# Kernel optimization log

Hardware: AMD Instinct MI355X
Metric: run time of the kernel (lower is better)

The kernel has to match this reference:

```python
import jax, jax.numpy as jnp
import numpy as np

EPS = 1e-5
H = 16  # num_heads


def _ln(x, s, b):
    m = x.mean(-1, keepdims=True)
    v = x.var(-1, keepdims=True)
    return (x - m) / jnp.sqrt(v + EPS) * s + b


def _gru_gate(x, y, W, U, bg):
    # W, U: [3, D, D] stacked (Wr, Wz, Wg) / (Ur, Uz, Ug); torch Linear: a @ W.T
    r = jax.nn.sigmoid(y @ W[0].T + x @ U[0].T)
    z = jax.nn.sigmoid(y @ W[1].T + x @ U[1].T - bg)
    h = jnp.tanh(y @ W[2].T + (r * x) @ U[2].T)
    return (1.0 - z) * x + z * h


def setup_inputs() -> dict:
    N, L, D = 4, 1024, 1024
    hs = D // H
    rng = jax.random.key(0)
    ks = iter(jax.random.split(rng, 24))

    def xav(shape):
        sc = float(np.sqrt(2.0 / (shape[-1] + shape[-2])))
        return jax.random.normal(next(ks), shape, jnp.float32) * sc

    inp = {
        'value': jax.random.normal(next(ks), (N, L, D), jnp.float32),
        'key': jax.random.normal(next(ks), (N, L, D), jnp.float32),
        'query': jax.random.normal(next(ks), (N, L, D), jnp.float32),
        'mask': jax.random.randint(next(ks), (N, L), 0, 2).astype(jnp.int32),
        # shared-head QKV projections (head_size x head_size)
        'wq': xav((hs, hs)), 'wk': xav((hs, hs)), 'wv': xav((hs, hs)),
        'w_out': xav((D, D)), 'b_out': jnp.zeros((D,), jnp.float32),
        'fc_w': xav((D, D)), 'fc_b': jnp.zeros((D,), jnp.float32),
        'ln1_s': jnp.ones((D,), jnp.float32), 'ln1_b': jnp.zeros((D,), jnp.float32),
        'lnkv_s': jnp.ones((D,), jnp.float32), 'lnkv_b': jnp.zeros((D,), jnp.float32),
        'ln2_s': jnp.ones((D,), jnp.float32), 'ln2_b': jnp.zeros((D,), jnp.float32),
        'g1_W': xav((3, D, D)), 'g1_U': xav((3, D, D)), 'g1_bg': jnp.full((D,), 2.0, jnp.float32),
        'g2_W': xav((3, D, D)), 'g2_U': xav((3, D, D)), 'g2_bg': jnp.full((D,), 2.0, jnp.float32),
    }
    return inp


def reference(value, key, query, mask, wq, wk, wv, w_out, b_out, fc_w, fc_b,
              ln1_s, ln1_b, lnkv_s, lnkv_b, ln2_s, ln2_b,
              g1_W, g1_U, g1_bg, g2_W, g2_U, g2_bg):
    N, L, D = query.shape
    hs = D // H
    # pre-LN: query normed with norm1, value normed with norm_kv; key := normed value
    q_ = _ln(query, ln1_s, ln1_b)
    v_ = _ln(value, lnkv_s, lnkv_b)
    k_ = v_
    # shared per-head projections: [N, L, H, hs] @ W.T
    qh = q_.reshape(N, L, H, hs) @ wq.T
    kh = k_.reshape(N, L, H, hs) @ wk.T
    vh = v_.reshape(N, L, H, hs) @ wv.T
    energy = jnp.einsum('nqhd,nkhd->nhqk', qh, kh)
    energy = jnp.where(mask[:, None, None, :] == 0, jnp.float32(-1e20), energy)
    # NOTE: original scales by sqrt(embed_dim), not sqrt(head_size)
    attn = jax.nn.softmax(energy / jnp.sqrt(jnp.float32(D)), axis=-1)
    o = jnp.einsum('nhqk,nkhd->nqhd', attn, vh).reshape(N, L, D) @ w_out.T + b_out
    # GRU-gated residuals (GTrXL)
    h = _gru_gate(query, o, g1_W, g1_U, g1_bg)
    h_ = _ln(h, ln2_s, ln2_b)
    f = jax.nn.relu(h_ @ fc_w.T + fc_b)
    out = _gru_gate(h, f, g2_W, g2_U, g2_bg)
    return out, attn
```

## Files before the change

kernel.cpp:

```cpp
#include <hip/hip_runtime.h>
#include <cstdint>
#include <cstddef>

#define N_ 4
#define L_ 1024
#define D_ 1024
#define H_ 16
#define HS_ 64
#define M_ (N_*L_)
#define DD_ (D_*D_)
#define MD_ ((size_t)M_*D_)

typedef unsigned short u16;
typedef __bf16 b16x8 __attribute__((ext_vector_type(8)));
typedef float f32x4 __attribute__((ext_vector_type(4)));

__device__ __forceinline__ float sigmoidf_(float x) { return 1.0f / (1.0f + __expf(-x)); }
__device__ __forceinline__ u16 f2bf(float f) {
    union { float f; uint32_t u; } c; c.f = f;
    uint32_t u = c.u;
    u += 0x7fffu + ((u >> 16) & 1u);
    return (u16)(u >> 16);
}

template<int AUX>
__device__ __forceinline__ void gl_lds16(const void* g, void* l) {
    auto gp = reinterpret_cast<const __attribute__((address_space(1))) unsigned int*>(
        reinterpret_cast<uintptr_t>(g));
    auto lp = reinterpret_cast<__attribute__((address_space(3))) unsigned int*>(
        reinterpret_cast<uintptr_t>(l));
    __builtin_amdgcn_global_load_lds(gp, lp, 16, 0, AUX);
}

__global__ __launch_bounds__(256) void prep_weights_kernel(
    const float* __restrict__ w_out, const float* __restrict__ fc_w,
    const float* __restrict__ wq, const float* __restrict__ wk, const float* __restrict__ wv,
    const float* __restrict__ g1W, const float* __restrict__ g1U,
    const float* __restrict__ g2W, const float* __restrict__ g2U,
    const float* __restrict__ query, u16* __restrict__ Xq,
    u16* __restrict__ ws0) {
    u16* Wop = ws0;
    u16* Wfc = ws0 + (size_t)DD_;
    u16* WQKV = ws0 + 2 * (size_t)DD_;
    u16* G1rz = WQKV + 16384;
    u16* G1h = G1rz + 4 * (size_t)DD_;
    u16* G2rz = G1h + 2 * (size_t)DD_;
    u16* G2h = G2rz + 4 * (size_t)DD_;
    int b = blockIdx.x, t = threadIdx.x;
    const float* src; u16* dst; size_t si, di;
    if (b < 512) {
        size_t f = (size_t)b * 2048 + t * 8; src = w_out; si = f; dst = Wop; di = f;
    } else if (b < 1024) {
        size_t f = (size_t)(b - 512) * 2048 + t * 8; src = fc_w; si = f; dst = Wfc; di = f;
    } else if (b < 1030) {
        size_t f = (size_t)(b - 1024) * 2048 + t * 8;
        int which = (int)(f >> 12); size_t off = f & 4095;
        src = which == 0 ? wq : (which == 1 ? wk : wv); si = off; dst = WQKV; di = f;
    } else if (b < 3078) {
        size_t f = (size_t)(b - 1030) * 2048 + t * 8;
        size_t row = f >> 11, k = f & 2047; size_t n2 = (row >= 1024) ? 1 : 0;
        src = (k < 1024) ? (g1W + n2 * DD_) : (g1U + n2 * DD_);
        si = (row & 1023) * 1024 + (k & 1023); dst = G1rz; di = f;
    } else if (b < 4102) {
        size_t f = (size_t)(b - 3078) * 2048 + t * 8;
        size_t row = f >> 11, k = f & 2047;
        src = (k < 1024) ? (g1W + 2 * (size_t)DD_) : (g1U + 2 * (size_t)DD_);
        si = row * 1024 + (k & 1023); dst = G1h; di = f;
    } else if (b < 6150) {
        size_t f = (size_t)(b - 4102) * 2048 + t * 8;
        size_t row = f >> 11, k = f & 2047; size_t n2 = (row >= 1024) ? 1 : 0;
        src = (k < 1024) ? (g2W + n2 * DD_) : (g2U + n2 * DD_);
        si = (row & 1023) * 1024 + (k & 1023); dst = G2rz; di = f;
    } else if (b < 7174) {
        size_t f = (size_t)(b - 6150) * 2048 + t * 8;
        size_t row = f >> 11, k = f & 2047;
        src = (k < 1024) ? (g2W + 2 * (size_t)DD_) : (g2U + 2 * (size_t)DD_);
        si = row * 1024 + (k & 1023); dst = G2h; di = f;
    } else {
        size_t f = (size_t)(b - 7174) * 2048 + t * 8;
        src = query; si = f; dst = Xq; di = f;
    }
    float4 a = *(const float4*)&src[si];
    float4 b4 = *(const float4*)&src[si + 4];
    u16 o[8] = { f2bf(a.x), f2bf(a.y), f2bf(a.z), f2bf(a.w),
                 f2bf(b4.x), f2bf(b4.y), f2bf(b4.z), f2bf(b4.w) };
    *(uint4*)&dst[di] = *(uint4*)o;
}

__global__ __launch_bounds__(256) void ln2in1_kernel(const float* __restrict__ x0, u16* __restrict__ y0,
                                                     const float* __restrict__ sc0, const float* __restrict__ bi0,
                                                     const float* __restrict__ x1, u16* __restrict__ y1,
                                                     const float* __restrict__ sc1, const float* __restrict__ bi1) {
    int row = blockIdx.x;
    const float* x = blockIdx.y ? x1 : x0;
    u16* y = blockIdx.y ? y1 : y0;
    const float* sc = blockIdx.y ? sc1 : sc0;
    const float* bi = blockIdx.y ? bi1 : bi0;
    const float* xr = x + (size_t)row * D_;
    int t = threadIdx.x;
    float4 v = *(const float4*)&xr[t * 4];
    float s = v.x + v.y + v.z + v.w;
    float q = v.x * v.x + v.y * v.y + v.z * v.z + v.w * v.w;
#pragma unroll
    for (int o = 32; o > 0; o >>= 1) { s += __shfl_xor(s, o); q += __shfl_xor(q, o); }
    __shared__ float ss[4], sq[4];
    int w = t >> 6;
    if ((t & 63) == 0) { ss[w] = s; sq[w] = q; }
    __syncthreads();
    s = ss[0] + ss[1] + ss[2] + ss[3];
    q = sq[0] + sq[1] + sq[2] + sq[3];
    float mean = s * (1.0f / D_);
    float var = q * (1.0f / D_) - mean * mean;
    float inv = rsqrtf(var + 1e-5f);
    float4 sv = *(const float4*)&sc[t * 4];
    float4 bv = *(const float4*)&bi[t * 4];
    u16 ov[4] = { f2bf((v.x - mean) * inv * sv.x + bv.x),
                  f2bf((v.y - mean) * inv * sv.y + bv.y),
                  f2bf((v.z - mean) * inv * sv.z + bv.z),
                  f2bf((v.w - mean) * inv * sv.w + bv.w) };
    *(ushort4*)&y[(size_t)row * D_ + t * 4] = *(ushort4*)ov;
}

__global__ __launch_bounds__(256) void ln_kernel(const float* __restrict__ x, u16* __restrict__ y,
                                                 const float* __restrict__ sc, const float* __restrict__ bi) {
    int row = blockIdx.x;
    const float* xr = x + (size_t)row * D_;
    int t = threadIdx.x;
    float4 v = *(const float4*)&xr[t * 4];
    float s = v.x + v.y + v.z + v.w;
    float q = v.x * v.x + v.y * v.y + v.z * v.z + v.w * v.w;
#pragma unroll
    for (int o = 32; o > 0; o >>= 1) { s += __shfl_xor(s, o); q += __shfl_xor(q, o); }
    __shared__ float ss[4], sq[4];
    int w = t >> 6;
    if ((t & 63) == 0) { ss[w] = s; sq[w] = q; }
    __syncthreads();
    s = ss[0] + ss[1] + ss[2] + ss[3];
    q = sq[0] + sq[1] + sq[2] + sq[3];
    float mean = s * (1.0f / D_);
    float var = q * (1.0f / D_) - mean * mean;
    float inv = rsqrtf(var + 1e-5f);
    float4 sv = *(const float4*)&sc[t * 4];
    float4 bv = *(const float4*)&bi[t * 4];
    u16 ov[4] = { f2bf((v.x - mean) * inv * sv.x + bv.x),
                  f2bf((v.y - mean) * inv * sv.y + bv.y),
                  f2bf((v.z - mean) * inv * sv.z + bv.z),
                  f2bf((v.w - mean) * inv * sv.w + bv.w) };
    *(ushort4*)&y[(size_t)row * D_ + t * 4] = *(ushort4*)ov;
}

__global__ __launch_bounds__(256) void proj_mfma_kernel(const u16* __restrict__ qbf,
                                                        const u16* __restrict__ vbf,
                                                        const u16* __restrict__ wqkv,
                                                        u16* __restrict__ qh, u16* __restrict__ kh,
                                                        u16* __restrict__ vt) {
    int t = threadIdx.x, w = t >> 6, l = t & 63;
    int lr = l & 15, lg = l >> 4;
    int rb = blockIdx.x, h = blockIdx.y;
    int n = rb >> 3, lbase = (rb & 7) * 128;
    const u16* wqp = wqkv;
    const u16* wkp = wqkv + 4096;
    const u16* wvp = wqkv + 8192;
    b16x8 wqf[4][2], wkf[4][2], wvf[4][2];
#pragma unroll
    for (int dt = 0; dt < 4; ++dt)
#pragma unroll
        for (int ks = 0; ks < 2; ++ks) {
            int a = (dt * 16 + lr) * 64 + ks * 32 + lg * 8;
            wqf[dt][ks] = *(const b16x8*)&wqp[a];
            wkf[dt][ks] = *(const b16x8*)&wkp[a];
            wvf[dt][ks] = *(const b16x8*)&wvp[a];
        }
#pragma unroll
    for (int rr = 0; rr < 2; ++rr) {
        int rt = w * 2 + rr;
        size_t grow = (size_t)(n * 1024 + lbase + rt * 16 + lr);
        b16x8 aq[2], av[2];
#pragma unroll
        for (int ks = 0; ks < 2; ++ks) {
            aq[ks] = *(const b16x8*)&qbf[grow * D_ + h * 64 + ks * 32 + lg * 8];
            av[ks] = *(const b16x8*)&vbf[grow * D_ + h * 64 + ks * 32 + lg * 8];
        }
#pragma unroll
        for (int dt = 0; dt < 4; ++dt) {
            f32x4 cq = (f32x4){0.f, 0.f, 0.f, 0.f};
            f32x4 ck = (f32x4){0.f, 0.f, 0.f, 0.f};
            f32x4 cv = (f32x4){0.f, 0.f, 0.f, 0.f};
            cq = __builtin_amdgcn_mfma_f32_16x16x32_bf16(aq[0], wqf[dt][0], cq, 0, 0, 0);
            cq = __builtin_amdgcn_mfma_f32_16x16x32_bf16(aq[1], wqf[dt][1], cq, 0, 0, 0);
            ck = __builtin_amdgcn_mfma_f32_16x16x32_bf16(av[0], wkf[dt][0], ck, 0, 0, 0);
            ck = __builtin_amdgcn_mfma_f32_16x16x32_bf16(av[1], wkf[dt][1], ck, 0, 0, 0);
            cv = __builtin_amdgcn_mfma_f32_16x16x32_bf16(wvf[dt][0], av[0], cv, 0, 0, 0);
            cv = __builtin_amdgcn_mfma_f32_16x16x32_bf16(wvf[dt][1], av[1], cv, 0, 0, 0);
#pragma unroll
            for (int r = 0; r < 4; ++r) {
                size_t orow = (size_t)(n * 1024 + lbase + rt * 16 + lg * 4 + r);
                qh[orow * D_ + h * 64 + dt * 16 + lr] = f2bf(cq[r]);
                kh[orow * D_ + h * 64 + dt * 16 + lr] = f2bf(ck[r]);
                vt[((size_t)(n * H_ + h) * 64 + dt * 16 + lg * 4 + r) * L_ + lbase + rt * 16 + lr] = f2bf(cv[r]);
            }
        }
    }
}

#define PSTR 1032
__global__ __launch_bounds__(512, 4) void qk_pv_kernel(const u16* __restrict__ qh,
                                                       const u16* __restrict__ kh,
                                                       const u16* __restrict__ vt,
                                                       const int* __restrict__ mask,
                                                       float* __restrict__ attn,
                                                       u16* __restrict__ obf) {
    __shared__ u16 P_lds[32 * PSTR];
    __shared__ float redA[32][4];
    __shared__ float redB[32][4];
    int t = threadIdx.x;
    int w = t >> 6, l = t & 63;
    int qsub = w & 1, kq = w >> 1;
    int q0 = blockIdx.x * 32;
    int h = blockIdx.y, n = blockIdx.z;
    int lr = l & 15, lg = l >> 4;

    size_t qrow = ((size_t)(n * L_ + q0 + qsub * 16 + lr) * H_ + h) * HS_;
    b16x8 aq0 = *(const b16x8*)&qh[qrow + lg * 8];
    b16x8 aq1 = *(const b16x8*)&qh[qrow + 32 + lg * 8];

    f32x4 c[16];
#pragma unroll
    for (int i = 0; i < 16; ++i) c[i] = (f32x4){0.f, 0.f, 0.f, 0.f};

    size_t kbase = ((size_t)(n * L_ + kq * 256 + lr) * H_ + h) * HS_ + lg * 8;
#pragma unroll
    for (int kt = 0; kt < 16; ++kt) {
        const u16* kp = &kh[kbase + (size_t)kt * 16 * D_];
        b16x8 bk0 = *(const b16x8*)&kp[0];
        b16x8 bk1 = *(const b16x8*)&kp[32];
        c[kt] = __builtin_amdgcn_mfma_f32_16x16x32_bf16(aq0, bk0, c[kt], 0, 0, 0);
        c[kt] = __builtin_amdgcn_mfma_f32_16x16x32_bf16(aq1, bk1, c[kt], 0, 0, 0);
    }

    const float scl = 0.03125f;
    int kcol = kq * 256 + lr;
    float rowmax[4] = { -1e30f, -1e30f, -1e30f, -1e30f };
#pragma unroll
    for (int kt = 0; kt < 16; ++kt) {
        int mk = mask[n * L_ + kcol + kt * 16];
#pragma unroll
        for (int r = 0; r < 4; ++r) {
            float s = (mk != 0) ? c[kt][r] * scl : -1e20f;
            c[kt][r] = s;
            rowmax[r] = fmaxf(rowmax[r], s);
        }
    }
#pragma unroll
    for (int o = 8; o > 0; o >>= 1)
#pragma unroll
        for (int r = 0; r < 4; ++r) rowmax[r] = fmaxf(rowmax[r], __shfl_xor(rowmax[r], o));

    int qrow4 = qsub * 16 + lg * 4;
    if (lr == 0) {
#pragma unroll
        for (int r = 0; r < 4; ++r) redA[qrow4 + r][kq] = rowmax[r];
    }
    __syncthreads();
#pragma unroll
    for (int r = 0; r < 4; ++r)
        rowmax[r] = fmaxf(fmaxf(redA[qrow4 + r][0], redA[qrow4 + r][1]),
                          fmaxf(redA[qrow4 + r][2], redA[qrow4 + r][3]));
    float rowsum[4] = { 0.f, 0.f, 0.f, 0.f };
#pragma unroll
    for (int kt = 0; kt < 16; ++kt)
#pragma unroll
        for (int r = 0; r < 4; ++r) {
            float e = __expf(c[kt][r] - rowmax[r]);
            c[kt][r] = e;
            rowsum[r] += e;
        }
#pragma unroll
    for (int o = 8; o > 0; o >>= 1)
#pragma unroll
        for (int r = 0; r < 4; ++r) rowsum[r] += __shfl_xor(rowsum[r], o);
    if (lr == 0) {
#pragma unroll
        for (int r = 0; r < 4; ++r) redB[qrow4 + r][kq] = rowsum[r];
    }
    __syncthreads();
    float inv[4];
#pragma unroll
    for (int r = 0; r < 4; ++r)
        inv[r] = 1.0f / (redB[qrow4 + r][0] + redB[qrow4 + r][1] +
                         redB[qrow4 + r][2] + redB[qrow4 + r][3]);

    float* ap = attn + ((size_t)((n * H_ + h) * L_) + q0 + qrow4) * L_ + kcol;
#pragma unroll
    for (int kt = 0; kt < 16; ++kt)
#pragma unroll
        for (int r = 0; r < 4; ++r) {
            float val = c[kt][r] * inv[r];
            __builtin_nontemporal_store(val, &ap[(size_t)r * L_ + kt * 16]);
            P_lds[(size_t)(qrow4 + r) * PSTR + kcol + kt * 16] = f2bf(val);
        }
    __syncthreads();

    int dg = kq;
    const u16* vb = vt + ((size_t)(n * H_ + h) * 64 + dg * 16 + lr) * L_;
    const u16* prow = &P_lds[(size_t)(qsub * 16 + lr) * PSTR];
    f32x4 acc = (f32x4){0.f, 0.f, 0.f, 0.f};
#pragma unroll
    for (int ks = 0; ks < 32; ++ks) {
        b16x8 a = *(const b16x8*)&prow[ks * 32 + lg * 8];
        b16x8 b = *(const b16x8*)&vb[ks * 32 + lg * 8];
        acc = __builtin_amdgcn_mfma_f32_16x16x32_bf16(a, b, acc, 0, 0, 0);
    }
#pragma unroll
    for (int r = 0; r < 4; ++r) {
        size_t q = (size_t)(n * L_ + q0 + qsub * 16 + lg * 4 + r);
        obf[q * D_ + h * 64 + dg * 16 + lr] = f2bf(acc[r]);
    }
}

template<int MODE, int RELU, int WRH>
__global__ __launch_bounds__(512, 4) void gemm_fused_kernel(const u16* __restrict__ A0,
                                                            const u16* __restrict__ A1h,
                                                            const u16* __restrict__ Bw,
                                                            const float* __restrict__ bias,
                                                            const float* __restrict__ xf,
                                                            float* __restrict__ Z,
                                                            u16* __restrict__ Cbf,
                                                            float* __restrict__ outf,
                                                            int K) {
    __shared__ u16 As[2][128 * 64];
    __shared__ u16 Bs[2][128 * 64];
    int t = threadIdx.x, w = t >> 6, l = t & 63;
    int wr = w & 3, wc = w >> 2;
    int flat = blockIdx.x;
    int xcd = flat & 7, idx = flat >> 3;
    int NP = gridDim.x >> 5;
    int ppx = NP >> 3;
    int panel = xcd * ppx + (idx >> 5);
    int mchunk = idx & 31;
    int m0 = mchunk * 128, n0 = panel * 128;
    int fr = l & 15, fq = l >> 4;
    int srow = l >> 3;
    int gc8 = (l & 7) ^ (srow & 7);
    const u16* Bbase = Bw + (size_t)n0 * K;

    f32x4 acc[2][4];
#pragma unroll
    for (int i = 0; i < 2; ++i)
#pragma unroll
        for (int j = 0; j < 4; ++j) acc[i][j] = (f32x4){0.f, 0.f, 0.f, 0.f};

    auto STAGE = [&](int buf, int kk) {
        const u16* Asrc = (MODE == 0 || kk < 1024) ? A0 : A1h;
        int kc = kk & 1023;
#pragma unroll
        for (int i = 0; i < 2; ++i) {
            int r0 = (i * 8 + w) * 8;
            gl_lds16<2>(&Asrc[(size_t)(m0 + r0 + srow) * 1024 + kc + gc8 * 8], &As[buf][r0 * 64]);
            gl_lds16<0>(&Bbase[(size_t)(r0 + srow) * K + kk + gc8 * 8], &Bs[buf][r0 * 64]);
        }
    };
    STAGE(0, 0);
    const int NT = K >> 6;
    for (int kt = 0; kt < NT; ++kt) {
        int cur = kt & 1;
        if (kt + 1 < NT) {
            STAGE(cur ^ 1, (kt + 1) << 6);
            asm volatile("s_waitcnt vmcnt(4)" ::: "memory");
        } else {
            asm volatile("s_waitcnt vmcnt(0)" ::: "memory");
        }
        __builtin_amdgcn_s_barrier();
#pragma unroll
        for (int ks = 0; ks < 2; ++ks) {
            b16x8 af[2], bf[4];
#pragma unroll
            for (int i = 0; i < 2; ++i) {
                int row = wr * 32 + i * 16 + fr;
                af[i] = *(const b16x8*)&As[cur][row * 64 + (((ks * 4 + fq) ^ (fr & 7)) * 8)];
            }
#pragma unroll
            for (int j = 0; j < 4; ++j) {
                int row = wc * 64 + j * 16 + fr;
                bf[j] = *(const b16x8*)&Bs[cur][row * 64 + (((ks * 4 + fq) ^ (fr & 7)) * 8)];
            }
#pragma unroll
            for (int i = 0; i < 2; ++i)
#pragma unroll
                for (int j = 0; j < 4; ++j)
                    acc[i][j] = __builtin_amdgcn_mfma_f32_16x16x32_bf16(af[i], bf[j], acc[i][j], 0, 0, 0);
        }
        asm volatile("s_waitcnt lgkmcnt(0)" ::: "memory");
        __builtin_amdgcn_s_barrier();
    }

#pragma unroll
    for (int i = 0; i < 2; ++i) {
#pragma unroll
        for (int j = 0; j < 4; ++j) {
            int row = m0 + wr * 32 + i * 16 + fq * 4;
            int col = n0 + wc * 64 + j * 16 + fr;
            int c1 = col & 1023;
#pragma unroll
            for (int r = 0; r < 4; ++r) {
                float v = acc[i][j][r];
                size_t off = (size_t)(row + r) * 1024 + c1;
                if (MODE == 0) {
                    v += bias[col];
                    if (RELU) v = fmaxf(v, 0.f);
                    Cbf[off] = f2bf(v);
                } else if (MODE == 1) {
                    if (col < 1024) Cbf[off] = f2bf(sigmoidf_(v) * xf[off]);
                    else            Z[off] = sigmoidf_(v - bias[c1]);
                } else {
                    float z = Z[off];
                    float o = (1.f - z) * xf[off] + z * tanhf(v);
                    outf[off] = o;
                    if (WRH) Cbf[off] = f2bf(o);
                }
            }
        }
    }
}

extern "C" void kernel_launch(void* const* d_in, const int* in_sizes, int n_in,
                              void* d_out, int out_size, void* d_ws, size_t ws_size,
                              hipStream_t stream) {
    const float* value = (const float*)d_in[0];
    const float* query = (const float*)d_in[2];
    const int* mask = (const int*)d_in[3];
    const float* wq = (const float*)d_in[4];
    const float* wk = (const float*)d_in[5];
    const float* wv = (const float*)d_in[6];
    const float* w_out = (const float*)d_in[7];
    const float* b_out = (const float*)d_in[8];
    const float* fc_w = (const float*)d_in[9];
    const float* fc_b = (const float*)d_in[10];
    const float* ln1_s = (const float*)d_in[11];
    const float* ln1_b = (const float*)d_in[12];
    const float* lnkv_s = (const float*)d_in[13];
    const float* lnkv_b = (const float*)d_in[14];
    const float* ln2_s = (const float*)d_in[15];
    const float* ln2_b = (const float*)d_in[16];
    const float* g1_W = (const float*)d_in[17];
    const float* g1_U = (const float*)d_in[18];
    const float* g1_bg = (const float*)d_in[19];
    const float* g2_W = (const float*)d_in[20];
    const float* g2_U = (const float*)d_in[21];
    const float* g2_bg = (const float*)d_in[22];

    float* out_f = (float*)d_out;
    float* attn_f = out_f + MD_;
    float* OutH = out_f;

    u16* WS = (u16*)d_ws;
    u16* Wop = WS;
    u16* Wfc = WS + (size_t)DD_;
    u16* WQKV = WS + 2 * (size_t)DD_;
    u16* G1rz = WQKV + 16384;
    u16* G1h  = G1rz + 4 * (size_t)DD_;
    u16* G2rz = G1h + 2 * (size_t)DD_;
    u16* G2h  = G2rz + 4 * (size_t)DD_;
    u16* Y    = G2h + 2 * (size_t)DD_;
    u16* Xq   = Y + MD_;
    u16* T1   = Xq + MD_;
    u16* Hb   = T1 + MD_;
    u16* F    = Hb + MD_;
    u16* QH   = F + MD_;
    u16* KH   = QH + MD_;
    u16* VT   = KH + MD_;
    u16* OBF  = VT + MD_;
    u16* LNQ  = OBF + MD_;
    u16* LNV  = LNQ + MD_;
    u16* LN2  = LNV + MD_;
    float* Z  = (float*)(LN2 + MD_);

    dim3 grid_n1024(256);
    dim3 grid_n2048(512);

    prep_weights_kernel<<<9222, 256, 0, stream>>>(w_out, fc_w, wq, wk, wv,
                                                  g1_W, g1_U, g2_W, g2_U, query, Xq, WS);

    ln2in1_kernel<<<dim3(M_, 2), 256, 0, stream>>>(query, LNQ, ln1_s, ln1_b,
                                                   value, LNV, lnkv_s, lnkv_b);
    proj_mfma_kernel<<<dim3(32, 16), 256, 0, stream>>>(LNQ, LNV, WQKV, QH, KH, VT);
    qk_pv_kernel<<<dim3(L_ / 32, H_, N_), 512, 0, stream>>>(QH, KH, VT, mask, attn_f, OBF);
    gemm_fused_kernel<0, 0, 0><<<grid_n1024, 512, 0, stream>>>(OBF, nullptr, Wop, b_out,
                                                               nullptr, nullptr, Y, nullptr, 1024);
    gemm_fused_kernel<1, 0, 0><<<grid_n2048, 512, 0, stream>>>(Y, Xq, G1rz, g1_bg,
                                                               query, Z, T1, nullptr, 2048);
    gemm_fused_kernel<2, 0, 1><<<grid_n1024, 512, 0, stream>>>(Y, T1, G1h, nullptr,
                                                               query, Z, Hb, OutH, 2048);
    ln_kernel<<<M_, 256, 0, stream>>>(OutH, LN2, ln2_s, ln2_b);
    gemm_fused_kernel<0, 1, 0><<<grid_n1024, 512, 0, stream>>>(LN2, nullptr, Wfc, fc_b,
                                                               nullptr, nullptr, F, nullptr, 1024);
    gemm_fused_kernel<1, 0, 0><<<grid_n2048, 512, 0, stream>>>(F, Hb, G2rz, g2_bg,
                                                               OutH, Z, T1, nullptr, 2048);
    gemm_fused_kernel<2, 0, 0><<<grid_n1024, 512, 0, stream>>>(F, T1, G2h, nullptr,
                                                               OutH, Z, nullptr, out_f, 2048);
}
```

Before: 446.8 us.

## Use bf16 for gate residual and Z buffers, simplify GEMM grid mapping

The GRU gate epilogues now read the residual input x and the z gate from bf16 copies (Xq, Hb, a bf16 Z buffer) instead of fp32 query, OutH and an fp32 Z. This halves the epilogue memory traffic. The change also drops the XCD-aware block swizzle in favour of a plain 2D grid, removes the cache-policy aux bits on the global-to-LDS loads, and replaces the nontemporal attention-probability stores with ordinary stores. Residual precision loss from bf16 x and z may affect accuracy, and losing the swizzle may reduce L2 locality.

```diff
diff --git a/kernel.cpp b/kernel.cpp
--- a/kernel.cpp
+++ b/kernel.cpp
@@ -22,14 +22,16 @@
     u += 0x7fffu + ((u >> 16) & 1u);
     return (u16)(u >> 16);
 }
-
-template<int AUX>
+__device__ __forceinline__ float bf2f(u16 u) {
+    union { uint32_t u; float f; } c; c.u = ((uint32_t)u) << 16; return c.f;
+}
+
 __device__ __forceinline__ void gl_lds16(const void* g, void* l) {
     auto gp = reinterpret_cast<const __attribute__((address_space(1))) unsigned int*>(
         reinterpret_cast<uintptr_t>(g));
     auto lp = reinterpret_cast<__attribute__((address_space(3))) unsigned int*>(
         reinterpret_cast<uintptr_t>(l));
-    __builtin_amdgcn_global_load_lds(gp, lp, 16, 0, AUX);
+    __builtin_amdgcn_global_load_lds(gp, lp, 16, 0, 0);
 }
 
 __global__ __launch_bounds__(256) void prep_weights_kernel(
@@ -296,7 +298,7 @@
 #pragma unroll
         for (int r = 0; r < 4; ++r) {
             float val = c[kt][r] * inv[r];
-            __builtin_nontemporal_store(val, &ap[(size_t)r * L_ + kt * 16]);
+            ap[(size_t)r * L_ + kt * 16] = val;
             P_lds[(size_t)(qrow4 + r) * PSTR + kcol + kt * 16] = f2bf(val);
         }
     __syncthreads();
@@ -323,8 +325,8 @@
                                                             const u16* __restrict__ A1h,
                                                             const u16* __restrict__ Bw,
                                                             const float* __restrict__ bias,
-                                                            const float* __restrict__ xf,
-                                                            float* __restrict__ Z,
+                                                            const u16* __restrict__ Xbf,
+                                                            u16* __restrict__ Zbf,
                                                             u16* __restrict__ Cbf,
                                                             float* __restrict__ outf,
                                                             int K) {
@@ -332,13 +334,7 @@
     __shared__ u16 Bs[2][128 * 64];
     int t = threadIdx.x, w = t >> 6, l = t & 63;
     int wr = w & 3, wc = w >> 2;
-    int flat = blockIdx.x;
-    int xcd = flat & 7, idx = flat >> 3;
-    int NP = gridDim.x >> 5;
-    int ppx = NP >> 3;
-    int panel = xcd * ppx + (idx >> 5);
-    int mchunk = idx & 31;
-    int m0 = mchunk * 128, n0 = panel * 128;
+    int m0 = blockIdx.x * 128, n0 = blockIdx.y * 128;
     int fr = l & 15, fq = l >> 4;
     int srow = l >> 3;
     int gc8 = (l & 7) ^ (srow & 7);
@@ -356,8 +352,8 @@
 #pragma unroll
         for (int i = 0; i < 2; ++i) {
             int r0 = (i * 8 + w) * 8;
-            gl_lds16<2>(&Asrc[(size_t)(m0 + r0 + srow) * 1024 + kc + gc8 * 8], &As[buf][r0 * 64]);
-            gl_lds16<0>(&Bbase[(size_t)(r0 + srow) * K + kk + gc8 * 8], &Bs[buf][r0 * 64]);
+            gl_lds16(&Asrc[(size_t)(m0 + r0 + srow) * 1024 + kc + gc8 * 8], &As[buf][r0 * 64]);
+            gl_lds16(&Bbase[(size_t)(r0 + srow) * K + kk + gc8 * 8], &Bs[buf][r0 * 64]);
         }
     };
     STAGE(0, 0);
@@ -410,11 +406,11 @@
                     if (RELU) v = fmaxf(v, 0.f);
                     Cbf[off] = f2bf(v);
                 } else if (MODE == 1) {
-                    if (col < 1024) Cbf[off] = f2bf(sigmoidf_(v) * xf[off]);
-                    else            Z[off] = sigmoidf_(v - bias[c1]);
+                    if (col < 1024) Cbf[off] = f2bf(sigmoidf_(v) * bf2f(Xbf[off]));
+                    else            Zbf[off] = f2bf(sigmoidf_(v - bias[c1]));
                 } else {
-                    float z = Z[off];
-                    float o = (1.f - z) * xf[off] + z * tanhf(v);
+                    float z = bf2f(Zbf[off]);
+                    float o = (1.f - z) * bf2f(Xbf[off]) + z * tanhf(v);
                     outf[off] = o;
                     if (WRH) Cbf[off] = f2bf(o);
                 }
@@ -473,10 +469,10 @@
     u16* LNQ  = OBF + MD_;
     u16* LNV  = LNQ + MD_;
     u16* LN2  = LNV + MD_;
-    float* Z  = (float*)(LN2 + MD_);
-
-    dim3 grid_n1024(256);
-    dim3 grid_n2048(512);
+    u16* Zb   = LN2 + MD_;
+
+    dim3 grid_n1024(M_ / 128, 8);
+    dim3 grid_n2048(M_ / 128, 16);
 
     prep_weights_kernel<<<9222, 256, 0, stream>>>(w_out, fc_w, wq, wk, wv,
                                                   g1_W, g1_U, g2_W, g2_U, query, Xq, WS);
@@ -488,14 +484,14 @@
     gemm_fused_kernel<0, 0, 0><<<grid_n1024, 512, 0, stream>>>(OBF, nullptr, Wop, b_out,
                                                                nullptr, nullptr, Y, nullptr, 1024);
     gemm_fused_kernel<1, 0, 0><<<grid_n2048, 512, 0, stream>>>(Y, Xq, G1rz, g1_bg,
-                                                               query, Z, T1, nullptr, 2048);
+                                                               Xq, Zb, T1, nullptr, 2048);
     gemm_fused_kernel<2, 0, 1><<<grid_n1024, 512, 0, stream>>>(Y, T1, G1h, nullptr,
-                                                               query, Z, Hb, OutH, 2048);
+                                                               Xq, Zb, Hb, OutH, 2048);
     ln_kernel<<<M_, 256, 0, stream>>>(OutH, LN2, ln2_s, ln2_b);
     gemm_fused_kernel<0, 1, 0><<<grid_n1024, 512, 0, stream>>>(LN2, nullptr, Wfc, fc_b,
                                                                nullptr, nullptr, F, nullptr, 1024);
     gemm_fused_kernel<1, 0, 0><<<grid_n2048, 512, 0, stream>>>(F, Hb, G2rz, g2_bg,
-                                                               OutH, Z, T1, nullptr, 2048);
+                                                               Hb, Zb, T1, nullptr, 2048);
     gemm_fused_kernel<2, 0, 0><<<grid_n1024, 512, 0, stream>>>(F, T1, G2h, nullptr,
-                                                               OutH, Z, nullptr, out_f, 2048);
-}
+                                                               Hb, Zb, nullptr, out_f, 2048);
+}
```

Result: faster. 386.5 us, median of 3 (-13.5%).
